# Performance work log

Measured on AMD Instinct MI355X. Metric: run time of the kernel, lower is better.

## Reference

```python
import jax, jax.numpy as jnp
import numpy as np

D = 768  # feature_dim


def setup_inputs() -> dict:
    key = jax.random.key(0)
    ks = jax.random.split(key, 8)
    B, L = 8, 2048
    vision_features = jax.random.normal(ks[0], (B, L, D), dtype=jnp.float32)
    language_features = jax.random.normal(ks[1], (B, L, D), dtype=jnp.float32)
    s = 1.0 / np.sqrt(D)
    Wv = jax.random.uniform(ks[2], (D, D), jnp.float32, -s, s)
    bv = jax.random.uniform(ks[3], (D,), jnp.float32, -s, s)
    Wl = jax.random.uniform(ks[4], (D, D), jnp.float32, -s, s)
    bl = jax.random.uniform(ks[5], (D,), jnp.float32, -s, s)
    so = 1.0 / np.sqrt(2 * D)
    Wo = jax.random.uniform(ks[6], (D, 2 * D), jnp.float32, -so, so)
    bo = jax.random.uniform(ks[7], (D,), jnp.float32, -so, so)
    return {
        "vision_features": vision_features,
        "language_features": language_features,
        "Wv": Wv, "bv": bv, "Wl": Wl, "bl": bl, "Wo": Wo, "bo": bo,
    }


def reference(vision_features, language_features, Wv, bv, Wl, bl, Wo, bo):
    # linear projections (torch Linear: x @ W^T + b)
    vp = jnp.einsum('bld,ed->ble', vision_features, Wv) + bv      # [B,L,D]
    lp = jnp.einsum('bld,ed->ble', language_features, Wl) + bl    # [B,L,D]
    # unscaled bidirectional attention
    sim = jnp.einsum('bid,bjd->bij', vp, lp)                      # [B,L,L]
    attn = jax.nn.softmax(sim, axis=-1)
    aligned_vision = jnp.einsum('bij,bjd->bid', attn, vp)         # [B,L,D]
    aligned_language = jnp.einsum('bij,bid->bjd', attn, lp)       # attn^T @ lp -> [B,L,D]
    combined = jnp.concatenate([aligned_vision, aligned_language], axis=-1)  # [B,L,2D]
    return jnp.einsum('blc,ec->ble', combined, Wo) + bo           # [B,L,D]
```

## Files before the change

### kernel.cpp

```cpp
#include <hip/hip_runtime.h>
#include <stdint.h>

typedef __attribute__((ext_vector_type(8))) short bf16x8;
typedef __attribute__((ext_vector_type(4))) float f32x4;

__device__ __forceinline__ float b2f(short h) {
  return __uint_as_float(((unsigned)(unsigned short)h) << 16);
}
__device__ __forceinline__ short f2b(float f) {
  unsigned u = __float_as_uint(f);
  u += 0x7fffu + ((u >> 16) & 1u);
  return (short)(u >> 16);
}

__device__ __forceinline__ void glds16(const void* g, void* l) {
  __builtin_amdgcn_global_load_lds(
      (const __attribute__((address_space(1))) void*)g,
      (__attribute__((address_space(3))) void*)l, 16, 0, 0);
}

__device__ __forceinline__ void xcd_decode(int C, int RSX, int RPZ,
                                           int& z, int& rowB, int& colB) {
  int id = blockIdx.x;
  int xcd = id & 7, slot = id >> 3;
  int rs = xcd * RSX + slot / C;
  colB = (slot % C) * 128;
  z = rs / RPZ;
  rowB = (rs % RPZ) * 128;
}

__global__ __launch_bounds__(256) void rowsum_kernel(const short* __restrict__ P,
                                                     float* __restrict__ invL) {
  int wave = threadIdx.x >> 6, lane = threadIdx.x & 63;
  size_t row = (size_t)blockIdx.x * 4 + wave;
  const short* p = P + row * 2048;
  float s = 0.f;
#pragma unroll
  for (int it = 0; it < 4; ++it) {
    bf16x8 x = *reinterpret_cast<const bf16x8*>(&p[it * 512 + lane * 8]);
#pragma unroll
    for (int j = 0; j < 8; ++j) s += b2f(x[j]);
  }
#pragma unroll
  for (int m = 32; m; m >>= 1) s += __shfl_xor(s, m);
  if (lane == 0) invL[row] = 1.0f / s;
}

__global__ __launch_bounds__(256) void proj3_kernel(
    const float* __restrict__ Vf, const float* __restrict__ Lf,
    const float* __restrict__ Wv, const float* __restrict__ Wl,
    const float* __restrict__ bv, const float* __restrict__ bl,
    short* __restrict__ vp_hi, short* __restrict__ lp_hi, short* __restrict__ lp_lo) {
  __shared__ alignas(16) short AsH[128 * 32];
  __shared__ alignas(16) short AsL[128 * 32];
  __shared__ alignas(16) short BsH[128 * 32];
  __shared__ alignas(16) short BsL[128 * 32];
  const int tid = threadIdx.x;
  int z, rowBase, colBase;
  xcd_decode(6, 32, 128, z, rowBase, colBase);
  const float* Af = z ? Lf : Vf;
  const float* Bf = z ? Wl : Wv;
  const float* bias = z ? bl : bv;
  const int lane = tid & 63;
  const int ln = lane & 15;
  const int qd = lane >> 4;
  const int w = tid >> 6;
  const int wr = w >> 1, wc = w & 1;

  f32x4 acc[4][4];
#pragma unroll
  for (int i = 0; i < 4; ++i)
#pragma unroll
    for (int j = 0; j < 4; ++j) acc[i][j] = 0.f;

  for (int kb = 0; kb < 768; kb += 32) {
#pragma unroll
    for (int q = 0; q < 2; ++q) {
      int c = q * 256 + tid;
      int r = c >> 2;
      int k0 = (c & 3) << 3;
      int sw = k0 ^ ((r & 3) << 3);
      {
        const float* p = &Af[(size_t)(rowBase + r) * 768 + kb + k0];
        float4 v0 = *reinterpret_cast<const float4*>(p);
        float4 v1 = *reinterpret_cast<const float4*>(p + 4);
        float vv[8] = {v0.x, v0.y, v0.z, v0.w, v1.x, v1.y, v1.z, v1.w};
        bf16x8 th, tl;
#pragma unroll
        for (int s = 0; s < 8; ++s) {
          short h = f2b(vv[s]);
          th[s] = h;
          tl[s] = f2b(vv[s] - b2f(h));
        }
        *reinterpret_cast<bf16x8*>(&AsH[r * 32 + sw]) = th;
        *reinterpret_cast<bf16x8*>(&AsL[r * 32 + sw]) = tl;
      }
      {
        const float* p = &Bf[(size_t)(colBase + r) * 768 + kb + k0];
        float4 v0 = *reinterpret_cast<const float4*>(p);
        float4 v1 = *reinterpret_cast<const float4*>(p + 4);
        float vv[8] = {v0.x, v0.y, v0.z, v0.w, v1.x, v1.y, v1.z, v1.w};
        bf16x8 th, tl;
#pragma unroll
        for (int s = 0; s < 8; ++s) {
          short h = f2b(vv[s]);
          th[s] = h;
          tl[s] = f2b(vv[s] - b2f(h));
        }
        *reinterpret_cast<bf16x8*>(&BsH[r * 32 + sw]) = th;
        *reinterpret_cast<bf16x8*>(&BsL[r * 32 + sw]) = tl;
      }
    }
    __syncthreads();
    bf16x8 ah[4], bh[4], tf[4];
#pragma unroll
    for (int rt = 0; rt < 4; ++rt) {
      int m = wr * 64 + rt * 16 + ln;
      ah[rt] = *reinterpret_cast<const bf16x8*>(&AsH[m * 32 + ((qd * 8) ^ ((m & 3) << 3))]);
    }
#pragma unroll
    for (int ct = 0; ct < 4; ++ct) {
      int n = wc * 64 + ct * 16 + ln;
      bh[ct] = *reinterpret_cast<const bf16x8*>(&BsH[n * 32 + ((qd * 8) ^ ((n & 3) << 3))]);
    }
#pragma unroll
    for (int rt = 0; rt < 4; ++rt)
#pragma unroll
      for (int ct = 0; ct < 4; ++ct)
        acc[rt][ct] = __builtin_amdgcn_mfma_f32_16x16x32_bf16(ah[rt], bh[ct], acc[rt][ct], 0, 0, 0);
#pragma unroll
    for (int rt = 0; rt < 4; ++rt) {
      int m = wr * 64 + rt * 16 + ln;
      tf[rt] = *reinterpret_cast<const bf16x8*>(&AsL[m * 32 + ((qd * 8) ^ ((m & 3) << 3))]);
    }
#pragma unroll
    for (int rt = 0; rt < 4; ++rt)
#pragma unroll
      for (int ct = 0; ct < 4; ++ct)
        acc[rt][ct] = __builtin_amdgcn_mfma_f32_16x16x32_bf16(tf[rt], bh[ct], acc[rt][ct], 0, 0, 0);
#pragma unroll
    for (int ct = 0; ct < 4; ++ct) {
      int n = wc * 64 + ct * 16 + ln;
      tf[ct] = *reinterpret_cast<const bf16x8*>(&BsL[n * 32 + ((qd * 8) ^ ((n & 3) << 3))]);
    }
#pragma unroll
    for (int rt = 0; rt < 4; ++rt)
#pragma unroll
      for (int ct = 0; ct < 4; ++ct)
        acc[rt][ct] = __builtin_amdgcn_mfma_f32_16x16x32_bf16(ah[rt], tf[ct], acc[rt][ct], 0, 0, 0);
    __syncthreads();
  }

#pragma unroll
  for (int rt = 0; rt < 4; ++rt) {
    int row0 = rowBase + wr * 64 + rt * 16 + qd * 4;
#pragma unroll
    for (int ct = 0; ct < 4; ++ct) {
      int col = colBase + wc * 64 + ct * 16 + ln;
      float bb = bias[col];
      f32x4 a = acc[rt][ct];
      if (z == 0) {
#pragma unroll
        for (int r = 0; r < 4; ++r)
          vp_hi[(size_t)(row0 + r) * 768 + col] = f2b(a[r] + bb);
      } else {
#pragma unroll
        for (int r = 0; r < 4; ++r) {
          float val = a[r] + bb;
          short h = f2b(val);
          lp_hi[(size_t)(row0 + r) * 768 + col] = h;
          lp_lo[(size_t)(row0 + r) * 768 + col] = f2b(val - b2f(h));
        }
      }
    }
  }
}

__global__ __launch_bounds__(256) void sim2_kernel(const short* __restrict__ vp,
                                                   const short* __restrict__ lph,
                                                   const short* __restrict__ lpl,
                                                   short* __restrict__ P) {
  __shared__ alignas(16) short As[128 * 32];
  __shared__ alignas(16) short Bh[128 * 32];
  __shared__ alignas(16) short Bl[128 * 32];
  const int tid = threadIdx.x;
  int z, rowBase, colBase;
  xcd_decode(16, 16, 16, z, rowBase, colBase);
  const short* Az = vp + (size_t)z * 2048 * 768;
  const short* B0 = lph + (size_t)z * 2048 * 768;
  const short* B1 = lpl + (size_t)z * 2048 * 768;
  const int lane = tid & 63;
  const int ln = lane & 15;
  const int qd = lane >> 4;
  const int w = tid >> 6;
  const int wr = w >> 1, wc = w & 1;

  f32x4 acc[4][4];
#pragma unroll
  for (int i = 0; i < 4; ++i)
#pragma unroll
    for (int j = 0; j < 4; ++j) acc[i][j] = 0.f;

  for (int kb = 0; kb < 768; kb += 32) {
#pragma unroll
    for (int q = 0; q < 2; ++q) {
      int c = q * 256 + tid;
      int r = c >> 2;
      int k0 = (c & 3) << 3;
      glds16(&Az[(size_t)(rowBase + r) * 768 + kb + k0], &As[c * 8]);
      glds16(&B0[(size_t)(colBase + r) * 768 + kb + k0], &Bh[c * 8]);
      glds16(&B1[(size_t)(colBase + r) * 768 + kb + k0], &Bl[c * 8]);
    }
    __syncthreads();
    bf16x8 af[4], bf[4];
#pragma unroll
    for (int rt = 0; rt < 4; ++rt)
      af[rt] = *reinterpret_cast<const bf16x8*>(&As[(wr * 64 + rt * 16 + ln) * 32 + qd * 8]);
#pragma unroll
    for (int ct = 0; ct < 4; ++ct)
      bf[ct] = *reinterpret_cast<const bf16x8*>(&Bh[(wc * 64 + ct * 16 + ln) * 32 + qd * 8]);
#pragma unroll
    for (int rt = 0; rt < 4; ++rt)
#pragma unroll
      for (int ct = 0; ct < 4; ++ct)
        acc[rt][ct] = __builtin_amdgcn_mfma_f32_16x16x32_bf16(af[rt], bf[ct], acc[rt][ct], 0, 0, 0);
#pragma unroll
    for (int ct = 0; ct < 4; ++ct)
      bf[ct] = *reinterpret_cast<const bf16x8*>(&Bl[(wc * 64 + ct * 16 + ln) * 32 + qd * 8]);
#pragma unroll
    for (int rt = 0; rt < 4; ++rt)
#pragma unroll
      for (int ct = 0; ct < 4; ++ct)
        acc[rt][ct] = __builtin_amdgcn_mfma_f32_16x16x32_bf16(af[rt], bf[ct], acc[rt][ct], 0, 0, 0);
    __syncthreads();
  }

  short* Pz = P + (size_t)z * 2048 * 2048;
#pragma unroll
  for (int rt = 0; rt < 4; ++rt) {
    int row0 = rowBase + wr * 64 + rt * 16 + qd * 4;
#pragma unroll
    for (int ct = 0; ct < 4; ++ct) {
      int col = colBase + wc * 64 + ct * 16 + ln;
      f32x4 a = acc[rt][ct];
#pragma unroll
      for (int r = 0; r < 4; ++r)
        Pz[(size_t)(row0 + r) * 2048 + col] = f2b(__expf(a[r] - 20.0f));
    }
  }
}

template <int MODE, bool TA, bool TB, bool SB, bool BF32, bool DUALA>
__global__ __launch_bounds__(256) void gemm_k(const short* __restrict__ A,
                                              const short* __restrict__ A2,
                                              const void* __restrict__ B,
                                              void* __restrict__ C,
                                              const float* __restrict__ bias,
                                              const float* __restrict__ invL,
                                              int C_, int RSX_, int RPZ_,
                                              int K, int ldA, int ldB, int ldC,
                                              long sA, long sB, long sC, long sL) {
  __shared__ alignas(16) short As[128 * 32];
  __shared__ alignas(16) short Bs[128 * 32];
  const int tid = threadIdx.x;
  int z, rowBase, colBase;
  xcd_decode(C_, RSX_, RPZ_, z, rowBase, colBase);
  const short* Az = A + (size_t)z * sA;
  const float* Lz = invL ? (invL + (size_t)z * sL) : nullptr;
  const int lane = tid & 63;
  const int ln = lane & 15;
  const int qd = lane >> 4;
  const int w = tid >> 6;
  const int wr = w >> 1, wc = w & 1;
  constexpr bool GA = !TA;
  constexpr bool GB = !TB && !BF32;

  f32x4 acc[4][4];
#pragma unroll
  for (int i = 0; i < 4; ++i)
#pragma unroll
    for (int j = 0; j < 4; ++j) acc[i][j] = 0.f;

  for (int kb = 0; kb < K; kb += 32) {
    if constexpr (GA) {
#pragma unroll
      for (int q = 0; q < 2; ++q) {
        int c = q * 256 + tid;
        int r = c >> 2;
        int k0 = (c & 3) << 3;
        int kk = kb + k0;
        const short* src;
        if constexpr (DUALA) {
          src = (kk < 768) ? &Az[(size_t)(rowBase + r) * 768 + kk]
                           : &A2[(size_t)(rowBase + r) * 768 + kk - 768];
        } else {
          src = &Az[(size_t)(rowBase + r) * ldA + kk];
        }
        glds16(src, &As[c * 8]);
      }
    } else {
#pragma unroll
      for (int q = 0; q < 2; ++q) {
        int task = q * 256 + tid;
        int m = task & 127;
        int kc = (task >> 7) << 3;
        bf16x8 t;
#pragma unroll
        for (int s = 0; s < 8; ++s)
          t[s] = Az[(size_t)(kb + kc + s) * ldA + rowBase + m];
        *reinterpret_cast<bf16x8*>(&As[m * 32 + (kc ^ ((m & 3) << 3))]) = t;
      }
    }
    if constexpr (TB) {
      const short* Bz = (const short*)B + (size_t)z * sB;
#pragma unroll
      for (int q = 0; q < 2; ++q) {
        int task = q * 256 + tid;
        int n = task & 127;
        int kc = (task >> 7) << 3;
        bf16x8 t;
#pragma unroll
        for (int s = 0; s < 8; ++s) {
          short v = Bz[(size_t)(kb + kc + s) * ldB + colBase + n];
          if constexpr (SB) v = f2b(b2f(v) * Lz[kb + kc + s]);
          t[s] = v;
        }
        *reinterpret_cast<bf16x8*>(&Bs[n * 32 + (kc ^ ((n & 3) << 3))]) = t;
      }
    } else if constexpr (BF32) {
      const float* Bf = (const float*)B + (size_t)z * sB;
#pragma unroll
      for (int q = 0; q < 2; ++q) {
        int c = q * 256 + tid;
        int r = c >> 2;
        int k0 = (c & 3) << 3;
        const float* p = &Bf[(size_t)(colBase + r) * ldB + kb + k0];
        float4 v0 = *reinterpret_cast<const float4*>(p);
        float4 v1 = *reinterpret_cast<const float4*>(p + 4);
        float vv[8] = {v0.x, v0.y, v0.z, v0.w, v1.x, v1.y, v1.z, v1.w};
        bf16x8 t;
#pragma unroll
        for (int s = 0; s < 8; ++s) t[s] = f2b(vv[s]);
        *reinterpret_cast<bf16x8*>(&Bs[r * 32 + (k0 ^ ((r & 3) << 3))]) = t;
      }
    } else {
      const short* Bz = (const short*)B + (size_t)z * sB;
#pragma unroll
      for (int q = 0; q < 2; ++q) {
        int c = q * 256 + tid;
        int r = c >> 2;
        int k0 = (c & 3) << 3;
        glds16(&Bz[(size_t)(colBase + r) * ldB + kb + k0], &Bs[c * 8]);
      }
    }
    __syncthreads();
    bf16x8 af[4], bfv[4];
#pragma unroll
    for (int rt = 0; rt < 4; ++rt) {
      int m = wr * 64 + rt * 16 + ln;
      int off = GA ? (qd * 8) : ((qd * 8) ^ ((m & 3) << 3));
      af[rt] = *reinterpret_cast<const bf16x8*>(&As[m * 32 + off]);
    }
#pragma unroll
    for (int ct = 0; ct < 4; ++ct) {
      int n = wc * 64 + ct * 16 + ln;
      int off = GB ? (qd * 8) : ((qd * 8) ^ ((n & 3) << 3));
      bfv[ct] = *reinterpret_cast<const bf16x8*>(&Bs[n * 32 + off]);
    }
#pragma unroll
    for (int rt = 0; rt < 4; ++rt)
#pragma unroll
      for (int ct = 0; ct < 4; ++ct)
        acc[rt][ct] =
            __builtin_amdgcn_mfma_f32_16x16x32_bf16(af[rt], bfv[ct], acc[rt][ct], 0, 0, 0);
    __syncthreads();
  }

#pragma unroll
  for (int rt = 0; rt < 4; ++rt) {
    int row0 = rowBase + wr * 64 + rt * 16 + qd * 4;
#pragma unroll
    for (int ct = 0; ct < 4; ++ct) {
      int col = colBase + wc * 64 + ct * 16 + ln;
      f32x4 a = acc[rt][ct];
      if constexpr (MODE == 2) {
        short* Co = (short*)C + (size_t)z * sC;
#pragma unroll
        for (int r = 0; r < 4; ++r)
          Co[(size_t)(row0 + r) * ldC + col] = f2b(a[r] * Lz[row0 + r]);
      } else if constexpr (MODE == 3) {
        short* Co = (short*)C + (size_t)z * sC;
#pragma unroll
        for (int r = 0; r < 4; ++r) Co[(size_t)(row0 + r) * ldC + col] = f2b(a[r]);
      } else {
        float* Co = (float*)C + (size_t)z * sC;
        float bb = bias[col];
#pragma unroll
        for (int r = 0; r < 4; ++r) Co[(size_t)(row0 + r) * ldC + col] = a[r] + bb;
      }
    }
  }
}

extern "C" void kernel_launch(void* const* d_in, const int* in_sizes, int n_in,
                              void* d_out, int out_size, void* d_ws, size_t ws_size,
                              hipStream_t stream) {
  const float* vf = (const float*)d_in[0];
  const float* lf = (const float*)d_in[1];
  const float* Wv = (const float*)d_in[2];
  const float* bv = (const float*)d_in[3];
  const float* Wl = (const float*)d_in[4];
  const float* bl = (const float*)d_in[5];
  const float* Wo = (const float*)d_in[6];
  const float* bo = (const float*)d_in[7];

  constexpr int Bz = 8, L = 2048, D = 768, M = Bz * L, D2 = 2 * D;
  constexpr size_t PLANE = (size_t)M * D;

  char* wp = (char*)d_ws;
  auto alloc = [&](size_t bytes) {
    char* p = wp;
    wp += (bytes + 255) & ~(size_t)255;
    return p;
  };
  short* vp_hi = (short*)alloc(PLANE * 2);
  short* P     = (short*)alloc((size_t)Bz * L * L * 2);
  float* invL  = (float*)alloc((size_t)M * 4);
  short* al      = vp_hi;
  float* out_tmp = (float*)P;

  short* lp_hi = (short*)d_out;
  short* lp_lo = lp_hi + PLANE;
  short* av    = lp_lo;

  proj3_kernel<<<dim3(1536), 256, 0, stream>>>(vf, lf, Wv, Wl, bv, bl, vp_hi, lp_hi, lp_lo);

  sim2_kernel<<<dim3(2048), 256, 0, stream>>>(vp_hi, lp_hi, lp_lo, P);

  rowsum_kernel<<<dim3(M / 4), 256, 0, stream>>>(P, invL);

  gemm_k<2, false, true, false, false, false><<<dim3(768), 256, 0, stream>>>(
      P, nullptr, vp_hi, av, nullptr, invL, 6, 16, 16, L, L, D, D,
      (long)L * L, (long)L * D, (long)L * D, (long)L);

  gemm_k<3, true, true, true, false, false><<<dim3(768), 256, 0, stream>>>(
      P, nullptr, lp_hi, al, nullptr, invL, 6, 16, 16, L, L, D, D,
      (long)L * L, (long)L * D, (long)L * D, (long)L);

  gemm_k<4, false, false, false, true, true><<<dim3(768), 256, 0, stream>>>(
      av, al, Wo, out_tmp, bo, nullptr, 6, 16, 128, D2, D, D2, D, 0, 0, 0, 0);

  hipMemcpyAsync(d_out, out_tmp, (size_t)M * D * 4, hipMemcpyDeviceToDevice, stream);
}
```

Measured before the change: 694.5 us.

## Pre-split fp32 inputs to bf16 hi/lo planes and load projection tiles via LDS DMA

Adds a conversion kernel that splits the fp32 features and weights into bf16 hi/lo planes once, staged in the P workspace. The projection GEMM then loads these planes straight into shared memory with global_load_lds instead of converting fp32 inside every tile, so the repeated per-tile conversion of weights and activations goes away. The single fused projection launch becomes two, one each for the vision and language sides. The cost is extra global traffic for the intermediate planes, more kernel launches, and dropping the LDS XOR swizzle, which may cause bank conflicts.

New measurement: 697.5 us. No clear change (+0.4%).

```diff
diff --git a/kernel.cpp b/kernel.cpp
--- a/kernel.cpp
+++ b/kernel.cpp
@@ -29,6 +29,44 @@
   rowB = (rs % RPZ) * 128;
 }
 
+__global__ __launch_bounds__(256) void cvt_kernel(
+    const float* __restrict__ S0, short* __restrict__ H0, short* __restrict__ L0,
+    const float* __restrict__ S1, short* __restrict__ H1, short* __restrict__ L1,
+    const float* __restrict__ S2, short* __restrict__ H2, short* __restrict__ L2,
+    int n0, int n1, int n2) {
+  int g = blockIdx.x * 256 + threadIdx.x;
+  const float* s;
+  short* h;
+  short* l;
+  if (g < n0) {
+    s = S0 + (size_t)g * 8;
+    h = H0 + (size_t)g * 8;
+    l = L0 + (size_t)g * 8;
+  } else if (g < n0 + n1) {
+    size_t t = (size_t)(g - n0);
+    s = S1 + t * 8;
+    h = H1 + t * 8;
+    l = L1 + t * 8;
+  } else {
+    size_t t = (size_t)(g - n0 - n1);
+    s = S2 + t * 8;
+    h = H2 + t * 8;
+    l = L2 + t * 8;
+  }
+  float4 v0 = *reinterpret_cast<const float4*>(s);
+  float4 v1 = *reinterpret_cast<const float4*>(s + 4);
+  float vv[8] = {v0.x, v0.y, v0.z, v0.w, v1.x, v1.y, v1.z, v1.w};
+  bf16x8 th, tl;
+#pragma unroll
+  for (int j = 0; j < 8; ++j) {
+    short hh = f2b(vv[j]);
+    th[j] = hh;
+    tl[j] = f2b(vv[j] - b2f(hh));
+  }
+  *reinterpret_cast<bf16x8*>(h) = th;
+  *reinterpret_cast<bf16x8*>(l) = tl;
+}
+
 __global__ __launch_bounds__(256) void rowsum_kernel(const short* __restrict__ P,
                                                      float* __restrict__ invL) {
   int wave = threadIdx.x >> 6, lane = threadIdx.x & 63;
@@ -46,21 +84,20 @@
   if (lane == 0) invL[row] = 1.0f / s;
 }
 
-__global__ __launch_bounds__(256) void proj3_kernel(
-    const float* __restrict__ Vf, const float* __restrict__ Lf,
-    const float* __restrict__ Wv, const float* __restrict__ Wl,
-    const float* __restrict__ bv, const float* __restrict__ bl,
-    short* __restrict__ vp_hi, short* __restrict__ lp_hi, short* __restrict__ lp_lo) {
+template <bool LO>
+__global__ __launch_bounds__(256) void projg_kernel(
+    const short* __restrict__ Ah, const short* __restrict__ Al,
+    const short* __restrict__ Bh, const short* __restrict__ Bl,
+    const float* __restrict__ bias,
+    short* __restrict__ Ch, short* __restrict__ Cl) {
   __shared__ alignas(16) short AsH[128 * 32];
   __shared__ alignas(16) short AsL[128 * 32];
   __shared__ alignas(16) short BsH[128 * 32];
   __shared__ alignas(16) short BsL[128 * 32];
   const int tid = threadIdx.x;
   int z, rowBase, colBase;
-  xcd_decode(6, 32, 128, z, rowBase, colBase);
-  const float* Af = z ? Lf : Vf;
-  const float* Bf = z ? Wl : Wv;
-  const float* bias = z ? bl : bv;
+  xcd_decode(6, 16, 128, z, rowBase, colBase);
+  (void)z;
   const int lane = tid & 63;
   const int ln = lane & 15;
   const int qd = lane >> 4;
@@ -79,75 +116,42 @@
       int c = q * 256 + tid;
       int r = c >> 2;
       int k0 = (c & 3) << 3;
-      int sw = k0 ^ ((r & 3) << 3);
-      {
-        const float* p = &Af[(size_t)(rowBase + r) * 768 + kb + k0];
-        float4 v0 = *reinterpret_cast<const float4*>(p);
-        float4 v1 = *reinterpret_cast<const float4*>(p + 4);
-        float vv[8] = {v0.x, v0.y, v0.z, v0.w, v1.x, v1.y, v1.z, v1.w};
-        bf16x8 th, tl;
-#pragma unroll
-        for (int s = 0; s < 8; ++s) {
-          short h = f2b(vv[s]);
-          th[s] = h;
-          tl[s] = f2b(vv[s] - b2f(h));
-        }
-        *reinterpret_cast<bf16x8*>(&AsH[r * 32 + sw]) = th;
-        *reinterpret_cast<bf16x8*>(&AsL[r * 32 + sw]) = tl;
-      }
-      {
-        const float* p = &Bf[(size_t)(colBase + r) * 768 + kb + k0];
-        float4 v0 = *reinterpret_cast<const float4*>(p);
-        float4 v1 = *reinterpret_cast<const float4*>(p + 4);
-        float vv[8] = {v0.x, v0.y, v0.z, v0.w, v1.x, v1.y, v1.z, v1.w};
-        bf16x8 th, tl;
-#pragma unroll
-        for (int s = 0; s < 8; ++s) {
-          short h = f2b(vv[s]);
-          th[s] = h;
-          tl[s] = f2b(vv[s] - b2f(h));
-        }
-        *reinterpret_cast<bf16x8*>(&BsH[r * 32 + sw]) = th;
-        *reinterpret_cast<bf16x8*>(&BsL[r * 32 + sw]) = tl;
-      }
-    }
-    __syncthreads();
-    bf16x8 ah[4], bh[4], tf[4];
-#pragma unroll
-    for (int rt = 0; rt < 4; ++rt) {
-      int m = wr * 64 + rt * 16 + ln;
-      ah[rt] = *reinterpret_cast<const bf16x8*>(&AsH[m * 32 + ((qd * 8) ^ ((m & 3) << 3))]);
-    }
-#pragma unroll
-    for (int ct = 0; ct < 4; ++ct) {
-      int n = wc * 64 + ct * 16 + ln;
-      bh[ct] = *reinterpret_cast<const bf16x8*>(&BsH[n * 32 + ((qd * 8) ^ ((n & 3) << 3))]);
-    }
+      size_t ao = (size_t)(rowBase + r) * 768 + kb + k0;
+      size_t bo = (size_t)(colBase + r) * 768 + kb + k0;
+      glds16(&Ah[ao], &AsH[c * 8]);
+      glds16(&Al[ao], &AsL[c * 8]);
+      glds16(&Bh[bo], &BsH[c * 8]);
+      glds16(&Bl[bo], &BsL[c * 8]);
+    }
+    __syncthreads();
+    bf16x8 ah[4], bh[4], t[4];
+#pragma unroll
+    for (int rt = 0; rt < 4; ++rt)
+      ah[rt] = *reinterpret_cast<const bf16x8*>(&AsH[(wr * 64 + rt * 16 + ln) * 32 + qd * 8]);
+#pragma unroll
+    for (int ct = 0; ct < 4; ++ct)
+      bh[ct] = *reinterpret_cast<const bf16x8*>(&BsH[(wc * 64 + ct * 16 + ln) * 32 + qd * 8]);
 #pragma unroll
     for (int rt = 0; rt < 4; ++rt)
 #pragma unroll
       for (int ct = 0; ct < 4; ++ct)
         acc[rt][ct] = __builtin_amdgcn_mfma_f32_16x16x32_bf16(ah[rt], bh[ct], acc[rt][ct], 0, 0, 0);
 #pragma unroll
-    for (int rt = 0; rt < 4; ++rt) {
-      int m = wr * 64 + rt * 16 + ln;
-      tf[rt] = *reinterpret_cast<const bf16x8*>(&AsL[m * 32 + ((qd * 8) ^ ((m & 3) << 3))]);
-    }
-#pragma unroll
-    for (int rt = 0; rt < 4; ++rt)
-#pragma unroll
-      for (int ct = 0; ct < 4; ++ct)
-        acc[rt][ct] = __builtin_amdgcn_mfma_f32_16x16x32_bf16(tf[rt], bh[ct], acc[rt][ct], 0, 0, 0);
-#pragma unroll
-    for (int ct = 0; ct < 4; ++ct) {
-      int n = wc * 64 + ct * 16 + ln;
-      tf[ct] = *reinterpret_cast<const bf16x8*>(&BsL[n * 32 + ((qd * 8) ^ ((n & 3) << 3))]);
-    }
-#pragma unroll
-    for (int rt = 0; rt < 4; ++rt)
-#pragma unroll
-      for (int ct = 0; ct < 4; ++ct)
-        acc[rt][ct] = __builtin_amdgcn_mfma_f32_16x16x32_bf16(ah[rt], tf[ct], acc[rt][ct], 0, 0, 0);
+    for (int rt = 0; rt < 4; ++rt)
+      t[rt] = *reinterpret_cast<const bf16x8*>(&AsL[(wr * 64 + rt * 16 + ln) * 32 + qd * 8]);
+#pragma unroll
+    for (int rt = 0; rt < 4; ++rt)
+#pragma unroll
+      for (int ct = 0; ct < 4; ++ct)
+        acc[rt][ct] = __builtin_amdgcn_mfma_f32_16x16x32_bf16(t[rt], bh[ct], acc[rt][ct], 0, 0, 0);
+#pragma unroll
+    for (int ct = 0; ct < 4; ++ct)
+      t[ct] = *reinterpret_cast<const bf16x8*>(&BsL[(wc * 64 + ct * 16 + ln) * 32 + qd * 8]);
+#pragma unroll
+    for (int rt = 0; rt < 4; ++rt)
+#pragma unroll
+      for (int ct = 0; ct < 4; ++ct)
+        acc[rt][ct] = __builtin_amdgcn_mfma_f32_16x16x32_bf16(ah[rt], t[ct], acc[rt][ct], 0, 0, 0);
     __syncthreads();
   }
 
@@ -159,18 +163,12 @@
       int col = colBase + wc * 64 + ct * 16 + ln;
       float bb = bias[col];
       f32x4 a = acc[rt][ct];
-      if (z == 0) {
-#pragma unroll
-        for (int r = 0; r < 4; ++r)
-          vp_hi[(size_t)(row0 + r) * 768 + col] = f2b(a[r] + bb);
-      } else {
-#pragma unroll
-        for (int r = 0; r < 4; ++r) {
-          float val = a[r] + bb;
-          short h = f2b(val);
-          lp_hi[(size_t)(row0 + r) * 768 + col] = h;
-          lp_lo[(size_t)(row0 + r) * 768 + col] = f2b(val - b2f(h));
-        }
+#pragma unroll
+      for (int r = 0; r < 4; ++r) {
+        float val = a[r] + bb;
+        short h = f2b(val);
+        Ch[(size_t)(row0 + r) * 768 + col] = h;
+        if constexpr (LO) Cl[(size_t)(row0 + r) * 768 + col] = f2b(val - b2f(h));
       }
     }
   }
@@ -416,6 +414,7 @@
 
   constexpr int Bz = 8, L = 2048, D = 768, M = Bz * L, D2 = 2 * D;
   constexpr size_t PLANE = (size_t)M * D;
+  constexpr size_t WPLANE = (size_t)D * D;
 
   char* wp = (char*)d_ws;
   auto alloc = [&](size_t bytes) {
@@ -433,7 +432,25 @@
   short* lp_lo = lp_hi + PLANE;
   short* av    = lp_lo;
 
-  proj3_kernel<<<dim3(1536), 256, 0, stream>>>(vf, lf, Wv, Wl, bv, bl, vp_hi, lp_hi, lp_lo);
+  short* fh  = P;
+  short* fl  = P + PLANE;
+  short* wvh = P + 2 * PLANE;
+  short* wvl = wvh + WPLANE;
+  short* wlh = wvl + WPLANE;
+  short* wll = wlh + WPLANE;
+
+  constexpr int GF = (int)(PLANE / 8);
+  constexpr int GW = (int)(WPLANE / 8);
+
+  cvt_kernel<<<dim3((GF + 2 * GW) / 256), 256, 0, stream>>>(
+      vf, fh, fl, Wv, wvh, wvl, Wl, wlh, wll, GF, GW, GW);
+
+  projg_kernel<false><<<dim3(768), 256, 0, stream>>>(fh, fl, wvh, wvl, bv, vp_hi, nullptr);
+
+  cvt_kernel<<<dim3(GF / 256), 256, 0, stream>>>(
+      lf, fh, fl, nullptr, nullptr, nullptr, nullptr, nullptr, nullptr, GF, 0, 0);
+
+  projg_kernel<true><<<dim3(768), 256, 0, stream>>>(fh, fl, wlh, wll, bl, lp_hi, lp_lo);
 
   sim2_kernel<<<dim3(2048), 256, 0, stream>>>(vp_hi, lp_hi, lp_lo, P);
 
```
